# Performance work log

Measured on AMD Instinct MI355X. Metric: run time of the kernel, lower is better.

## Reference

```python
import jax, jax.numpy as jnp
import numpy as np

NX, NY, D, K = 20000, 50000, 64, 8
NUM_BATCHES = 2


def _knn_np(px, py, bx, by, k):
    # Batched exact kNN via chunked squared-distance + argpartition (mirrors torch_cluster.knn under no_grad).
    pp = (px * px).sum(1)
    idx = np.empty((py.shape[0], k), np.int32)
    chunk = 4096
    for s in range(0, py.shape[0], chunk):
        q = py[s:s + chunk]
        d = (q * q).sum(1)[:, None] + pp[None, :] - 2.0 * (q @ px.T)
        d = np.where(by[s:s + chunk, None] == bx[None, :], d, np.inf)
        idx[s:s + chunk] = np.argpartition(d, k, axis=1)[:, :k].astype(np.int32)
    return idx


def setup_inputs() -> dict:
    rng = np.random.default_rng(0)
    pos_x = (rng.random((NX, 3)) * 10.0).astype(np.float32)
    pos_y = (rng.random((NY, 3)) * 10.0).astype(np.float32)
    bx = np.repeat(np.arange(NUM_BATCHES), NX // NUM_BATCHES).astype(np.int32)
    by = np.repeat(np.arange(NUM_BATCHES), NY // NUM_BATCHES).astype(np.int32)
    x_idx = _knn_np(pos_x, pos_y, bx, by, K).reshape(-1)            # [NY*K]
    y_idx = np.repeat(np.arange(NY, dtype=np.int32), K)             # [NY*K]

    key = jax.random.key(0)
    ks = jax.random.split(key, 6)

    def lin(k, fi, fo):
        return jax.random.normal(k, (fi, fo), jnp.float32) / np.sqrt(fi).astype(np.float32)

    return {
        "x": jax.random.normal(ks[0], (NX, D), jnp.float32),
        "pos_x": jnp.asarray(pos_x),
        "pos_y": jnp.asarray(pos_y),
        "x_idx": jnp.asarray(x_idx),
        "y_idx": jnp.asarray(y_idx),
        # ResnetBlockFC 1: size_in=D+3, size_h=D, size_out=D (shortcut linear, no bias)
        "W0a": lin(ks[1], D + 3, D), "b0a": jnp.zeros((D,), jnp.float32),
        "W1a": lin(ks[2], D, D),     "b1a": jnp.zeros((D,), jnp.float32),
        "Wsa": lin(ks[3], D + 3, D),
        # ResnetBlockFC 2: size_in=size_h=size_out=D (identity shortcut)
        "W0b": lin(ks[4], D, D),     "b0b": jnp.zeros((D,), jnp.float32),
        "W1b": lin(ks[5], D, D),     "b1b": jnp.zeros((D,), jnp.float32),
    }


def reference(x, pos_x, pos_y, x_idx, y_idx, W0a, b0a, W1a, b1a, Wsa, W0b, b0b, W1b, b1b):
    # gather + positional diff (diff computed under no_grad in the original)
    diff = jax.lax.stop_gradient(pos_x[x_idx] - pos_y[y_idx])        # [E, 3]
    h = jnp.concatenate([x[x_idx], diff], axis=1)                    # [E, D+3]
    # ResnetBlockFC 1: out = shortcut(h) + fc1(relu(fc0(relu(h))))
    net = jax.nn.relu(h) @ W0a + b0a
    dx = jax.nn.relu(net) @ W1a + b1a
    h = h @ Wsa + dx                                                 # [E, D]
    # ResnetBlockFC 2 (identity shortcut)
    net = jax.nn.relu(h) @ W0b + b0b
    h = h + jax.nn.relu(net) @ W1b + b1b                             # [E, D]
    # scatter-max back to query points (every query has exactly K edges)
    out = jax.ops.segment_max(h, y_idx, num_segments=NY)             # [NY, D]
    return out
```

## Files before the change

kernel.cpp:

```cpp
#include <hip/hip_runtime.h>


typedef _Float16 f16x8 __attribute__((ext_vector_type(8)));
typedef _Float16 f16x4 __attribute__((ext_vector_type(4)));
typedef float    f32x4 __attribute__((ext_vector_type(4)));

constexpr int NX     = 20000;
constexpr int NROWS  = 50000 * 8;
constexpr int NTILES = NROWS / 16;
constexpr int NFRAG  = 60;
constexpr int BW     = 8;
constexpr int BLOCK  = 64 * BW;
constexpr int TS2    = 72;

__global__ void prep_x(const float* __restrict__ x, _Float16* __restrict__ x16) {
    const int i = blockIdx.x * blockDim.x + threadIdx.x;
    if (i < NX * 16) {
        float4 v = ((const float4*)x)[i];
        f16x4 o = {(_Float16)v.x, (_Float16)v.y, (_Float16)v.z, (_Float16)v.w};
        *(f16x4*)(x16 + (size_t)i * 4) = o;
    }
}

static __device__ __forceinline__ void pack_relu(const f32x4* A, f16x8* bf) {
#pragma unroll
    for (int s = 0; s < 2; ++s) {
        f16x8 r;
#pragma unroll
        for (int e = 0; e < 8; ++e) {
            float v = A[2 * s + (e >> 2)][e & 3];
            r[e] = (_Float16)(v > 0.0f ? v : 0.0f);
        }
        bf[s] = r;
    }
}

__global__ __launch_bounds__(BLOCK, 4)
void pointnet_fused(const _Float16* __restrict__ x16,
                    const float* __restrict__ pos_x,
                    const float* __restrict__ pos_y,
                    const int*   __restrict__ x_idx,
                    const float* __restrict__ W0a, const float* __restrict__ b0a,
                    const float* __restrict__ W1a, const float* __restrict__ b1a,
                    const float* __restrict__ Wsa,
                    const float* __restrict__ W0b, const float* __restrict__ b0b,
                    const float* __restrict__ W1b, const float* __restrict__ b1b,
                    float* __restrict__ out)
{
    __shared__ __align__(16) _Float16 bfrag[NFRAG * 64 * 8];
    __shared__ __align__(16) _Float16 ebuf[BW][16 * TS2];

    const int tid = threadIdx.x;

    for (int p = tid; p < NFRAG * 64; p += BLOCK) {
        const int f = p >> 6, l = p & 63;
        const int q = l >> 4, n0 = l & 15;
        const int grp = f / 12, fl = f % 12, s = fl >> 2, t = fl & 3;
        const int col = t * 16 + n0;
        f16x8 v;
#pragma unroll
        for (int j = 0; j < 8; ++j) {
            const int k = 32 * s + 8 * q + j;
            float val = 0.0f;
            if (grp == 0)      val = (k < 67) ? W0a[k * 64 + col] : (k == 67 ? b0a[col] : 0.0f);
            else if (grp == 1) val = (k < 67) ? Wsa[k * 64 + col] : 0.0f;
            else {
                const float* W  = (grp == 2) ? W1a : (grp == 3) ? W0b : W1b;
                const float* bb = (grp == 2) ? b1a : (grp == 3) ? b0b : b1b;
                if (s < 2) {
                    const int row = 32 * s + 16 * (j >> 2) + 4 * q + (j & 3);
                    val = W[row * 64 + col];
                } else {
                    val = (q == 0 && j == 0) ? bb[col] : 0.0f;
                }
            }
            v[j] = (_Float16)val;
        }
        *(f16x8*)&bfrag[p * 8] = v;
    }
    __syncthreads();

    const int lane = tid & 63;
    const int wv   = tid >> 6;
    const int n0   = lane & 15;
    const int q    = lane >> 4;

    _Float16* eb = ebuf[wv];

    f16x8 bfr = {};
    if (q == 0) bfr[0] = (_Float16)1.0f;

    const int ey  = (lane >> 3) & 1;
    const int efg = lane & 7;
    const int esb = lane >> 4;

    const int gwave  = blockIdx.x * BW + wv;
    const int nwaves = gridDim.x * BW;

#define WFRAG(fid) (*(const f16x8*)&bfrag[(((fid) * 64) + lane) * 8])

    for (int tile = gwave; tile < NTILES; tile += nwaves) {
        const int row = tile * 16 + n0;
        const int xi  = x_idx[row];
        const _Float16* xp = x16 + (long)xi * 64 + q * 8;
        f16x8 hn[3];
        hn[0] = *(const f16x8*)(xp);
        hn[1] = *(const f16x8*)(xp + 32);
        {
            f16x8 z = {};
            hn[2] = z;
            if (q == 0) {
                const int yi = row >> 3;
#pragma unroll
                for (int j = 0; j < 3; ++j)
                    hn[2][j] = (_Float16)(pos_x[xi * 3 + j] - pos_y[yi * 3 + j]);
                hn[2][3] = (_Float16)1.0f;
            }
        }

        f32x4 A2[4];
#pragma unroll
        for (int t = 0; t < 4; ++t) A2[t] = (f32x4){0.f, 0.f, 0.f, 0.f};
#pragma unroll
        for (int s = 0; s < 3; ++s)
#pragma unroll
            for (int t = 0; t < 4; ++t)
                A2[t] = __builtin_amdgcn_mfma_f32_16x16x32_f16(WFRAG(12 + s * 4 + t), hn[s], A2[t], 0, 0, 0);

#pragma unroll
        for (int s = 0; s < 3; ++s)
#pragma unroll
            for (int j = 0; j < 8; ++j) {
                _Float16 v = hn[s][j];
                hn[s][j] = v > (_Float16)0 ? v : (_Float16)0;
            }
        f32x4 A1[4];
#pragma unroll
        for (int t = 0; t < 4; ++t) A1[t] = (f32x4){0.f, 0.f, 0.f, 0.f};
#pragma unroll
        for (int s = 0; s < 3; ++s)
#pragma unroll
            for (int t = 0; t < 4; ++t)
                A1[t] = __builtin_amdgcn_mfma_f32_16x16x32_f16(WFRAG(s * 4 + t), hn[s], A1[t], 0, 0, 0);

        f16x8 bf[2];
        pack_relu(A1, bf);
#pragma unroll
        for (int t = 0; t < 4; ++t) {
            A2[t] = __builtin_amdgcn_mfma_f32_16x16x32_f16(WFRAG(24 + 0 * 4 + t), bf[0], A2[t], 0, 0, 0);
            A2[t] = __builtin_amdgcn_mfma_f32_16x16x32_f16(WFRAG(24 + 1 * 4 + t), bf[1], A2[t], 0, 0, 0);
            A2[t] = __builtin_amdgcn_mfma_f32_16x16x32_f16(WFRAG(24 + 2 * 4 + t), bfr,   A2[t], 0, 0, 0);
        }

        pack_relu(A2, bf);
        f32x4 A3[4];
#pragma unroll
        for (int t = 0; t < 4; ++t) A3[t] = (f32x4){0.f, 0.f, 0.f, 0.f};
#pragma unroll
        for (int t = 0; t < 4; ++t) {
            A3[t] = __builtin_amdgcn_mfma_f32_16x16x32_f16(WFRAG(36 + 0 * 4 + t), bf[0], A3[t], 0, 0, 0);
            A3[t] = __builtin_amdgcn_mfma_f32_16x16x32_f16(WFRAG(36 + 1 * 4 + t), bf[1], A3[t], 0, 0, 0);
            A3[t] = __builtin_amdgcn_mfma_f32_16x16x32_f16(WFRAG(36 + 2 * 4 + t), bfr,   A3[t], 0, 0, 0);
        }

        pack_relu(A3, bf);
#pragma unroll
        for (int t = 0; t < 4; ++t) {
            A2[t] = __builtin_amdgcn_mfma_f32_16x16x32_f16(WFRAG(48 + 0 * 4 + t), bf[0], A2[t], 0, 0, 0);
            A2[t] = __builtin_amdgcn_mfma_f32_16x16x32_f16(WFRAG(48 + 1 * 4 + t), bf[1], A2[t], 0, 0, 0);
            A2[t] = __builtin_amdgcn_mfma_f32_16x16x32_f16(WFRAG(48 + 2 * 4 + t), bfr,   A2[t], 0, 0, 0);
        }

        __threadfence_block();
#pragma unroll
        for (int t = 0; t < 4; ++t) {
            f16x4 w;
#pragma unroll
            for (int r = 0; r < 4; ++r) w[r] = (_Float16)A2[t][r];
            *(f16x4*)&eb[n0 * TS2 + t * 16 + q * 4] = w;
        }
        __threadfence_block();

        const int dr0 = ey * 8 + esb * 2;
        f16x8 ra = *(const f16x8*)&eb[dr0 * TS2 + efg * 8];
        f16x8 rb = *(const f16x8*)&eb[(dr0 + 1) * TS2 + efg * 8];
#pragma unroll
        for (int e = 0; e < 8; ++e) ra[e] = ra[e] > rb[e] ? ra[e] : rb[e];
#pragma unroll
        for (int st = 0; st < 2; ++st) {
            union { f16x8 h; int i[4]; } u, v2;
            u.h = ra;
#pragma unroll
            for (int d = 0; d < 4; ++d) v2.i[d] = __shfl_xor(u.i[d], st == 0 ? 16 : 32, 64);
#pragma unroll
            for (int e = 0; e < 8; ++e) ra[e] = ra[e] > v2.h[e] ? ra[e] : v2.h[e];
        }
        if (esb == 0) {
            float4 f0 = {(float)ra[0], (float)ra[1], (float)ra[2], (float)ra[3]};
            float4 f1 = {(float)ra[4], (float)ra[5], (float)ra[6], (float)ra[7]};
            float* op = out + (long)(tile * 2 + ey) * 64 + efg * 8;
            *(float4*)op = f0;
            *(float4*)(op + 4) = f1;
        }
    }
#undef WFRAG
}

extern "C" void kernel_launch(void* const* d_in, const int* in_sizes, int n_in,
                              void* d_out, int out_size, void* d_ws, size_t ws_size,
                              hipStream_t stream) {
    (void)in_sizes; (void)n_in; (void)ws_size; (void)out_size;
    _Float16* x16 = (_Float16*)d_ws;

    prep_x<<<(NX * 16 + 255) / 256, 256, 0, stream>>>((const float*)d_in[0], x16);

    pointnet_fused<<<512, BLOCK, 0, stream>>>(
        x16,
        (const float*)d_in[1],
        (const float*)d_in[2],
        (const int*)  d_in[3],
        (const float*)d_in[5],  (const float*)d_in[6],
        (const float*)d_in[7],  (const float*)d_in[8],
        (const float*)d_in[9],
        (const float*)d_in[10], (const float*)d_in[11],
        (const float*)d_in[12], (const float*)d_in[13],
        (float*)d_out);
}
```

Measured before the change: 122.1 us.

## Prefetch next tile's gather and fold biases out of MFMA K-padding

Software-pipelines the per-tile gather so the next tile's x16 row, x_idx and position values are loaded while the current tile's MFMAs run, hiding global-memory latency. Removes the bias-only third K-slice from the three 64x64 layers: b1a is folded into the Wsa padding row, b0b initialises the accumulator from shared memory, and b1b is added after the segment max. The A1 and A2 first-layer MFMAs are interleaved. This cuts 12 MFMAs per tile and shrinks shared weight fragments, at the cost of extra registers for the prefetched tile, which may lower occupancy.

Result: no change. 124.1 us (+1.6%).

```diff
diff --git a/kernel.cpp b/kernel.cpp
--- a/kernel.cpp
+++ b/kernel.cpp
@@ -8,7 +8,7 @@
 constexpr int NX     = 20000;
 constexpr int NROWS  = 50000 * 8;
 constexpr int NTILES = NROWS / 16;
-constexpr int NFRAG  = 60;
+constexpr int NFRAG  = 48;
 constexpr int BW     = 8;
 constexpr int BLOCK  = 64 * BW;
 constexpr int TS2    = 72;
@@ -49,35 +49,40 @@
 {
     __shared__ __align__(16) _Float16 bfrag[NFRAG * 64 * 8];
     __shared__ __align__(16) _Float16 ebuf[BW][16 * TS2];
+    __shared__ __align__(16) float    bias3f[64];
+    __shared__ __align__(16) float    bias5f[64];
 
     const int tid = threadIdx.x;
 
     for (int p = tid; p < NFRAG * 64; p += BLOCK) {
         const int f = p >> 6, l = p & 63;
         const int q = l >> 4, n0 = l & 15;
-        const int grp = f / 12, fl = f % 12, s = fl >> 2, t = fl & 3;
+        int grp, fl;
+        if      (f < 12) { grp = 0; fl = f; }
+        else if (f < 24) { grp = 1; fl = f - 12; }
+        else if (f < 32) { grp = 2; fl = f - 24; }
+        else if (f < 40) { grp = 3; fl = f - 32; }
+        else             { grp = 4; fl = f - 40; }
+        const int s = fl >> 2, t = fl & 3;
         const int col = t * 16 + n0;
         f16x8 v;
 #pragma unroll
         for (int j = 0; j < 8; ++j) {
             const int k = 32 * s + 8 * q + j;
             float val = 0.0f;
-            if (grp == 0)      val = (k < 67) ? W0a[k * 64 + col] : (k == 67 ? b0a[col] : 0.0f);
-            else if (grp == 1) val = (k < 67) ? Wsa[k * 64 + col] : 0.0f;
+            if      (grp == 0) val = (k < 67) ? W0a[k * 64 + col] : (k == 67 ? b0a[col] : 0.0f);
+            else if (grp == 1) val = (k < 67) ? Wsa[k * 64 + col] : (k == 67 ? b1a[col] : 0.0f);
             else {
-                const float* W  = (grp == 2) ? W1a : (grp == 3) ? W0b : W1b;
-                const float* bb = (grp == 2) ? b1a : (grp == 3) ? b0b : b1b;
-                if (s < 2) {
-                    const int row = 32 * s + 16 * (j >> 2) + 4 * q + (j & 3);
-                    val = W[row * 64 + col];
-                } else {
-                    val = (q == 0 && j == 0) ? bb[col] : 0.0f;
-                }
+                const float* W = (grp == 2) ? W1a : (grp == 3) ? W0b : W1b;
+                const int row = 32 * s + 16 * (j >> 2) + 4 * q + (j & 3);
+                val = W[row * 64 + col];
             }
             v[j] = (_Float16)val;
         }
         *(f16x8*)&bfrag[p * 8] = v;
     }
+    if (tid < 64)       bias3f[tid]      = b0b[tid];
+    else if (tid < 128) bias5f[tid - 64] = b1b[tid - 64];
     __syncthreads();
 
     const int lane = tid & 63;
@@ -87,9 +92,6 @@
 
     _Float16* eb = ebuf[wv];
 
-    f16x8 bfr = {};
-    if (q == 0) bfr[0] = (_Float16)1.0f;
-
     const int ey  = (lane >> 3) & 1;
     const int efg = lane & 7;
     const int esb = lane >> 4;
@@ -99,77 +101,96 @@
 
 #define WFRAG(fid) (*(const f16x8*)&bfrag[(((fid) * 64) + lane) * 8])
 
-    for (int tile = gwave; tile < NTILES; tile += nwaves) {
-        const int row = tile * 16 + n0;
+    f16x8 hc0, hc1, hc2;
+    {
+        const int row = gwave * 16 + n0;
         const int xi  = x_idx[row];
         const _Float16* xp = x16 + (long)xi * 64 + q * 8;
-        f16x8 hn[3];
-        hn[0] = *(const f16x8*)(xp);
-        hn[1] = *(const f16x8*)(xp + 32);
+        hc0 = *(const f16x8*)(xp);
+        hc1 = *(const f16x8*)(xp + 32);
+        f16x8 z = {}; hc2 = z;
+        if (q == 0) {
+            const int yi = row >> 3;
+#pragma unroll
+            for (int j = 0; j < 3; ++j)
+                hc2[j] = (_Float16)(pos_x[xi * 3 + j] - pos_y[yi * 3 + j]);
+            hc2[3] = (_Float16)1.0f;
+        }
+    }
+
+    for (int tile = gwave; tile < NTILES; tile += nwaves) {
+        const int tnx  = tile + nwaves;
+        const int rown = (tnx < NTILES ? tnx : tile) * 16 + n0;
+        const int xin  = x_idx[rown];
+        const int yin  = rown >> 3;
+        const float py0 = pos_y[yin * 3 + 0];
+        const float py1 = pos_y[yin * 3 + 1];
+        const float py2 = pos_y[yin * 3 + 2];
+
+        f16x8 hr0 = hc0, hr1 = hc1, hr2 = hc2;
+#pragma unroll
+        for (int j = 0; j < 8; ++j) {
+            hr0[j] = hr0[j] > (_Float16)0 ? hr0[j] : (_Float16)0;
+            hr1[j] = hr1[j] > (_Float16)0 ? hr1[j] : (_Float16)0;
+            hr2[j] = hr2[j] > (_Float16)0 ? hr2[j] : (_Float16)0;
+        }
+
+        f32x4 A1[4], A2[4];
+#pragma unroll
+        for (int t = 0; t < 4; ++t) {
+            A1[t] = (f32x4){0.f, 0.f, 0.f, 0.f};
+            A2[t] = (f32x4){0.f, 0.f, 0.f, 0.f};
+        }
         {
-            f16x8 z = {};
-            hn[2] = z;
+            const f16x8 hcs[3] = {hc0, hc1, hc2};
+            const f16x8 hrs[3] = {hr0, hr1, hr2};
+#pragma unroll
+            for (int s = 0; s < 3; ++s)
+#pragma unroll
+                for (int t = 0; t < 4; ++t) {
+                    A2[t] = __builtin_amdgcn_mfma_f32_16x16x32_f16(WFRAG(12 + s * 4 + t), hcs[s], A2[t], 0, 0, 0);
+                    A1[t] = __builtin_amdgcn_mfma_f32_16x16x32_f16(WFRAG( 0 + s * 4 + t), hrs[s], A1[t], 0, 0, 0);
+                }
+        }
+
+        f16x8 hn0, hn1, hn2;
+        {
+            const _Float16* xp = x16 + (long)xin * 64 + q * 8;
+            hn0 = *(const f16x8*)(xp);
+            hn1 = *(const f16x8*)(xp + 32);
+            f16x8 z = {}; hn2 = z;
             if (q == 0) {
-                const int yi = row >> 3;
-#pragma unroll
-                for (int j = 0; j < 3; ++j)
-                    hn[2][j] = (_Float16)(pos_x[xi * 3 + j] - pos_y[yi * 3 + j]);
-                hn[2][3] = (_Float16)1.0f;
+                hn2[0] = (_Float16)(pos_x[xin * 3 + 0] - py0);
+                hn2[1] = (_Float16)(pos_x[xin * 3 + 1] - py1);
+                hn2[2] = (_Float16)(pos_x[xin * 3 + 2] - py2);
+                hn2[3] = (_Float16)1.0f;
             }
         }
-
-        f32x4 A2[4];
-#pragma unroll
-        for (int t = 0; t < 4; ++t) A2[t] = (f32x4){0.f, 0.f, 0.f, 0.f};
-#pragma unroll
-        for (int s = 0; s < 3; ++s)
-#pragma unroll
-            for (int t = 0; t < 4; ++t)
-                A2[t] = __builtin_amdgcn_mfma_f32_16x16x32_f16(WFRAG(12 + s * 4 + t), hn[s], A2[t], 0, 0, 0);
-
-#pragma unroll
-        for (int s = 0; s < 3; ++s)
-#pragma unroll
-            for (int j = 0; j < 8; ++j) {
-                _Float16 v = hn[s][j];
-                hn[s][j] = v > (_Float16)0 ? v : (_Float16)0;
-            }
-        f32x4 A1[4];
-#pragma unroll
-        for (int t = 0; t < 4; ++t) A1[t] = (f32x4){0.f, 0.f, 0.f, 0.f};
-#pragma unroll
-        for (int s = 0; s < 3; ++s)
-#pragma unroll
-            for (int t = 0; t < 4; ++t)
-                A1[t] = __builtin_amdgcn_mfma_f32_16x16x32_f16(WFRAG(s * 4 + t), hn[s], A1[t], 0, 0, 0);
 
         f16x8 bf[2];
         pack_relu(A1, bf);
 #pragma unroll
-        for (int t = 0; t < 4; ++t) {
-            A2[t] = __builtin_amdgcn_mfma_f32_16x16x32_f16(WFRAG(24 + 0 * 4 + t), bf[0], A2[t], 0, 0, 0);
-            A2[t] = __builtin_amdgcn_mfma_f32_16x16x32_f16(WFRAG(24 + 1 * 4 + t), bf[1], A2[t], 0, 0, 0);
-            A2[t] = __builtin_amdgcn_mfma_f32_16x16x32_f16(WFRAG(24 + 2 * 4 + t), bfr,   A2[t], 0, 0, 0);
-        }
+        for (int s = 0; s < 2; ++s)
+#pragma unroll
+            for (int t = 0; t < 4; ++t)
+                A2[t] = __builtin_amdgcn_mfma_f32_16x16x32_f16(WFRAG(24 + s * 4 + t), bf[s], A2[t], 0, 0, 0);
 
         pack_relu(A2, bf);
         f32x4 A3[4];
 #pragma unroll
-        for (int t = 0; t < 4; ++t) A3[t] = (f32x4){0.f, 0.f, 0.f, 0.f};
-#pragma unroll
-        for (int t = 0; t < 4; ++t) {
-            A3[t] = __builtin_amdgcn_mfma_f32_16x16x32_f16(WFRAG(36 + 0 * 4 + t), bf[0], A3[t], 0, 0, 0);
-            A3[t] = __builtin_amdgcn_mfma_f32_16x16x32_f16(WFRAG(36 + 1 * 4 + t), bf[1], A3[t], 0, 0, 0);
-            A3[t] = __builtin_amdgcn_mfma_f32_16x16x32_f16(WFRAG(36 + 2 * 4 + t), bfr,   A3[t], 0, 0, 0);
-        }
+        for (int t = 0; t < 4; ++t) A3[t] = *(const f32x4*)&bias3f[16 * t + 4 * q];
+#pragma unroll
+        for (int s = 0; s < 2; ++s)
+#pragma unroll
+            for (int t = 0; t < 4; ++t)
+                A3[t] = __builtin_amdgcn_mfma_f32_16x16x32_f16(WFRAG(32 + s * 4 + t), bf[s], A3[t], 0, 0, 0);
 
         pack_relu(A3, bf);
 #pragma unroll
-        for (int t = 0; t < 4; ++t) {
-            A2[t] = __builtin_amdgcn_mfma_f32_16x16x32_f16(WFRAG(48 + 0 * 4 + t), bf[0], A2[t], 0, 0, 0);
-            A2[t] = __builtin_amdgcn_mfma_f32_16x16x32_f16(WFRAG(48 + 1 * 4 + t), bf[1], A2[t], 0, 0, 0);
-            A2[t] = __builtin_amdgcn_mfma_f32_16x16x32_f16(WFRAG(48 + 2 * 4 + t), bfr,   A2[t], 0, 0, 0);
-        }
+        for (int s = 0; s < 2; ++s)
+#pragma unroll
+            for (int t = 0; t < 4; ++t)
+                A2[t] = __builtin_amdgcn_mfma_f32_16x16x32_f16(WFRAG(40 + s * 4 + t), bf[s], A2[t], 0, 0, 0);
 
         __threadfence_block();
 #pragma unroll
@@ -196,12 +217,18 @@
             for (int e = 0; e < 8; ++e) ra[e] = ra[e] > v2.h[e] ? ra[e] : v2.h[e];
         }
         if (esb == 0) {
-            float4 f0 = {(float)ra[0], (float)ra[1], (float)ra[2], (float)ra[3]};
-            float4 f1 = {(float)ra[4], (float)ra[5], (float)ra[6], (float)ra[7]};
+            const f32x4 bb0 = *(const f32x4*)&bias5f[efg * 8];
+            const f32x4 bb1 = *(const f32x4*)&bias5f[efg * 8 + 4];
+            float4 f0 = {(float)ra[0] + bb0[0], (float)ra[1] + bb0[1],
+                         (float)ra[2] + bb0[2], (float)ra[3] + bb0[3]};
+            float4 f1 = {(float)ra[4] + bb1[0], (float)ra[5] + bb1[1],
+                         (float)ra[6] + bb1[2], (float)ra[7] + bb1[3]};
             float* op = out + (long)(tile * 2 + ey) * 64 + efg * 8;
             *(float4*)op = f0;
             *(float4*)(op + 4) = f1;
         }
+
+        hc0 = hn0; hc1 = hn1; hc2 = hn2;
     }
 #undef WFRAG
 }
```
